# Performance work log

Hardware: AMD Instinct MI355X
Metric: run time of the kernel (lower is better)

The kernel has to match this reference:

```python
import jax, jax.numpy as jnp
import numpy as np
from jax import lax

BN_EPS = 1e-5


def setup_inputs() -> dict:
    key = jax.random.key(0)
    ks = jax.random.split(key, 12)
    h, c, i, kk = 8, 64, 96, 3
    c2, n, d = c // 2, 8, 512
    std = lambda f: np.float32(f)
    return {
        "X": jax.random.normal(ks[0], (h, n, d), jnp.float32),
        "lin_w": jax.random.normal(ks[1], (h, c2, d), jnp.float32) * std(d ** -0.5),
        "lin_b": jax.random.normal(ks[2], (h, c2), jnp.float32) * std(0.02),
        "bn_gamma": jnp.ones((h, c2), jnp.float32),
        "bn_beta": jnp.zeros((h, c2), jnp.float32),
        "px": jax.random.normal(ks[3], (1, 1, c2, 1, i), jnp.float32) * std(c ** -0.5),
        "py": jax.random.normal(ks[4], (1, 1, c2, i, 1), jnp.float32) * std(c ** -0.5),
        "kw": jax.random.normal(ks[5], (h, c, c), jnp.float32) * std(c ** -0.5),
        "kb": jax.random.normal(ks[6], (h, c), jnp.float32) * std(0.02),
        "vw": jax.random.normal(ks[7], (h, c, c), jnp.float32) * std(c ** -0.5),
        "vb": jax.random.normal(ks[8], (h, c), jnp.float32) * std(0.02),
        "sw": jax.random.normal(ks[9], (c, c, kk, kk), jnp.float32) * std((c * kk * kk) ** -0.5),
        "sb": jax.random.normal(ks[10], (c,), jnp.float32) * std(0.02),
    }


def reference(X, lin_w, lin_b, bn_gamma, bn_beta, px, py, kw, kb, vw, vb, sw, sb):
    h, n, _ = X.shape
    c = kw.shape[1]
    c2 = c // 2
    i = px.shape[-1]
    kk = sw.shape[-1]

    # --- MultiheadEmbedding: per-head Linear -> BatchNorm1d(train) -> ReLU ---
    y = jnp.einsum('hnd,hcd->hnc', X, lin_w) + lin_b[:, None, :]      # (h, n, c2)
    mu = y.mean(axis=1, keepdims=True)
    var = y.var(axis=1, keepdims=True)                                 # biased, as BN
    y = (y - mu) * lax.rsqrt(var + BN_EPS) * bn_gamma[:, None, :] + bn_beta[:, None, :]
    y = jax.nn.relu(y)
    M = jnp.transpose(y, (1, 0, 2))[..., None, None]                   # (n, h, c2, 1, 1)

    # --- PositionalEncoding: concat x/y translated copies -> (n, h, c, i, i) ---
    P = jnp.concatenate([
        jnp.broadcast_to(M + px, (n, h, c2, i, i)),
        jnp.broadcast_to(M + py, (n, h, c2, i, i)),
    ], axis=2)                                                          # (n, h, c, i, i)

    # --- TransposeAttention ---
    # grouped 1x1 key conv (groups = h)
    kp = jnp.einsum('nhcij,hdc->nhdij', P, kw) + kb[None, :, :, None, None]
    # score conv over each (c, i, i) map, shared across heads, scaled
    x = kp.reshape(n * h, c, i, i)
    s = lax.conv_general_dilated(x, sw, (1, 1), 'SAME',
                                 dimension_numbers=('NCHW', 'OIHW', 'NCHW'))
    s = (s + sb[None, :, None, None]) / np.float32((c * kk * kk) ** 0.5)
    w = jax.nn.softmax(s.reshape(n, h, c, i, i), axis=1)                # softmax over heads
    # grouped 1x1 value conv, weighted sum over heads
    vp = jnp.einsum('nhcij,hdc->nhdij', P, vw) + vb[None, :, :, None, None]
    T = (w * vp).sum(axis=1)                                            # (n, c, i, i)
    return (T, M, P, w)
```

## Files before the change

kernel.cpp:

```cpp
#include <hip/hip_runtime.h>
#include <math.h>

#define H    8
#define N    8
#define D    512
#define C    64
#define C2   32
#define I    96
#define II   9216

#define OFF_T 0
#define OFF_M 4718592
#define OFF_P 4720640
#define OFF_W 42469376

#define WS_AK 0
#define WS_AV 4096
#define WS_BK 8192
#define WS_BV 57344
#define WS_CK 106496
#define WS_CV 155648
#define WS_SS 204800
#define WS_SP 241664
#define WS_SQ 278528
#define WS_F  315392
#define WS_G2 352256
#define WS_H2 499712

__device__ __forceinline__ int bcls(int x) { return x == 0 ? 0 : (x == I - 1 ? 2 : 1); }

__global__ __launch_bounds__(256) void irf_embed(
    const float* __restrict__ X, const float* __restrict__ lin_w,
    const float* __restrict__ lin_b, const float* __restrict__ gamma,
    const float* __restrict__ beta, float* __restrict__ out)
{
    const int h = blockIdx.x, t = threadIdx.x;
    const int n = t >> 5, cc = t & 31;

    __shared__ float Xs[N * D];
    __shared__ float ys[N * C2];
    __shared__ float scale_s[C2], shift_s[C2];

    const float4* Xg  = (const float4*)(X + (size_t)h * N * D);
    float4*       Xs4 = (float4*)Xs;
    for (int idx = t; idx < N * D / 4; idx += 256) Xs4[idx] = Xg[idx];
    __syncthreads();

    const float4* wrow = (const float4*)(lin_w + ((size_t)h * C2 + cc) * D);
    const float4* xrow = (const float4*)(Xs + n * D);
    float a0 = 0.f, a1 = 0.f, a2 = 0.f, a3 = 0.f;
    #pragma unroll 4
    for (int k = 0; k < D / 4; ++k) {
        float4 xv = xrow[k], wv = wrow[k];
        a0 = fmaf(xv.x, wv.x, a0); a1 = fmaf(xv.y, wv.y, a1);
        a2 = fmaf(xv.z, wv.z, a2); a3 = fmaf(xv.w, wv.w, a3);
    }
    float y = (a0 + a1) + (a2 + a3) + lin_b[h * C2 + cc];
    ys[n * C2 + cc] = y;
    __syncthreads();

    if (t < C2) {
        float s = 0.f, ss = 0.f;
        #pragma unroll
        for (int j = 0; j < N; ++j) { float v = ys[j * C2 + t]; s += v; ss += v * v; }
        float mu  = s * (1.0f / N);
        float var = ss * (1.0f / N) - mu * mu;
        float sc  = rsqrtf(var + 1e-5f) * gamma[h * C2 + t];
        scale_s[t] = sc;
        shift_s[t] = beta[h * C2 + t] - mu * sc;
    }
    __syncthreads();

    float v = fmaxf(fmaf(y, scale_s[cc], shift_s[cc]), 0.0f);
    out[OFF_M + (n * H + h) * C2 + cc] = v;
}

__global__ __launch_bounds__(256) void irf_factors_a(
    const float* __restrict__ kw, const float* __restrict__ kb,
    const float* __restrict__ vw, const float* __restrict__ vb,
    const float* __restrict__ px, const float* __restrict__ py,
    const float* __restrict__ sw, const float* __restrict__ out,
    float* __restrict__ ws)
{
    int gid = blockIdx.x * 256 + threadIdx.x;
    if (gid < 4096) {
        int id = gid, d = id & 63, h = (id >> 6) & 7, n = id >> 9;
        const float* kwr = kw + ((size_t)h * C + d) * C;
        const float* vwr = vw + ((size_t)h * C + d) * C;
        const float* Mr  = out + OFF_M + (n * H + h) * C2;
        float ak = kb[h * C + d], av = vb[h * C + d];
        #pragma unroll 8
        for (int c = 0; c < C2; ++c) {
            float m = Mr[c];
            ak = fmaf(kwr[c] + kwr[C2 + c], m, ak);
            av = fmaf(vwr[c] + vwr[C2 + c], m, av);
        }
        ws[WS_AK + id] = ak;
        ws[WS_AV + id] = av;
    } else if (gid < 4096 + 49152) {
        int id = gid - 4096, d = id & 63, r = id >> 6, b = r % I, h = r / I;
        const float* kwr = kw + ((size_t)h * C + d) * C;
        const float* vwr = vw + ((size_t)h * C + d) * C;
        float bk = 0.f, bv = 0.f, ck = 0.f, cv = 0.f;
        #pragma unroll 8
        for (int c = 0; c < C2; ++c) {
            float pxv = px[c * I + b], pyv = py[c * I + b];
            bk = fmaf(kwr[c], pxv, bk);       bv = fmaf(vwr[c], pxv, bv);
            ck = fmaf(kwr[C2 + c], pyv, ck);  cv = fmaf(vwr[C2 + c], pyv, cv);
        }
        ws[WS_BK + id] = bk; ws[WS_BV + id] = bv;
        ws[WS_CK + id] = ck; ws[WS_CV + id] = cv;
    } else if (gid < 4096 + 49152 + 4096) {
        int id = gid - (4096 + 49152), d = id & 63, e = id >> 6;
        float k9[3][3];
        const float* swr = sw + (size_t)(e * C + d) * 9;
        #pragma unroll
        for (int p = 0; p < 3; ++p)
            #pragma unroll
            for (int q = 0; q < 3; ++q) k9[p][q] = swr[p * 3 + q];
        #pragma unroll
        for (int ra = 0; ra < 3; ++ra) {
            int pmin = (ra == 0) ? 1 : 0, pmax = (ra == 2) ? 1 : 2;
            #pragma unroll
            for (int q = 0; q < 3; ++q) {
                float sp = 0.f;
                for (int p = pmin; p <= pmax; ++p) sp += k9[p][q];
                ws[WS_SP + ((ra * 3 + q) * C + e) * C + d] = sp;
            }
            #pragma unroll
            for (int rb = 0; rb < 3; ++rb) {
                int qmin = (rb == 0) ? 1 : 0, qmax = (rb == 2) ? 1 : 2;
                float ssv = 0.f;
                for (int p = pmin; p <= pmax; ++p)
                    for (int q = qmin; q <= qmax; ++q) ssv += k9[p][q];
                ws[WS_SS + ((ra * 3 + rb) * C + e) * C + d] = ssv;
            }
        }
        #pragma unroll
        for (int rb = 0; rb < 3; ++rb) {
            int qmin = (rb == 0) ? 1 : 0, qmax = (rb == 2) ? 1 : 2;
            #pragma unroll
            for (int p = 0; p < 3; ++p) {
                float sq = 0.f;
                for (int q = qmin; q <= qmax; ++q) sq += k9[p][q];
                ws[WS_SQ + ((rb * 3 + p) * C + e) * C + d] = sq;
            }
        }
    }
}

__global__ __launch_bounds__(256) void irf_factors_b(float* __restrict__ ws)
{
    int gid = blockIdx.x * 256 + threadIdx.x;
    if (gid < 36864) {
        int id = gid, e = id & 63, h = (id >> 6) & 7, cls = (id >> 9) % 9, n = id / 4608;
        const float* ak = ws + WS_AK + (n * H + h) * C;
        const float* ss = ws + WS_SS + (cls * C + e) * C;
        float acc = 0.f;
        #pragma unroll 8
        for (int d = 0; d < C; ++d) acc = fmaf(ak[d], ss[d], acc);
        ws[WS_F + id] = acc;
    } else if (gid < 36864 + 147456) {
        int j = gid - 36864, b = j % I, e = (j / I) & 63, h = (j / (I * C)) & 7, ra = j / (I * C * H);
        int rb = bcls(b), qmin = (rb == 0) ? 1 : 0, qmax = (rb == 2) ? 1 : 2;
        float acc = 0.f;
        for (int q = qmin; q <= qmax; ++q) {
            const float* sp = ws + WS_SP + ((ra * 3 + q) * C + e) * C;
            const float* bk = ws + WS_BK + ((h * I) + (b + q - 1)) * C;
            #pragma unroll 8
            for (int d = 0; d < C; ++d) acc = fmaf(sp[d], bk[d], acc);
        }
        ws[WS_G2 + j] = acc;
    } else if (gid < 36864 + 2 * 147456) {
        int j = gid - 36864 - 147456, e = j & 63, h = (j >> 6) & 7, rb = (j >> 9) % 3, a = j / 1536;
        int ra = bcls(a), pmin = (ra == 0) ? 1 : 0, pmax = (ra == 2) ? 1 : 2;
        float acc = 0.f;
        for (int p = pmin; p <= pmax; ++p) {
            const float* sq = ws + WS_SQ + ((rb * 3 + p) * C + e) * C;
            const float* ck = ws + WS_CK + ((h * I) + (a + p - 1)) * C;
            #pragma unroll 8
            for (int d = 0; d < C; ++d) acc = fmaf(sq[d], ck[d], acc);
        }
        ws[WS_H2 + j] = acc;
    }
}

__global__ __launch_bounds__(256) void irf_site(
    const float* __restrict__ px, const float* __restrict__ py,
    const float* __restrict__ sb, const float* __restrict__ ws,
    float* __restrict__ out)
{
    const int bid = blockIdx.x;
    const int n = bid / I, a = bid - n * I;
    const int ra = bcls(a);
    const int t = threadIdx.x;
    const int e8 = t >> 5, bl = t & 31;

    __shared__ float Fs[3 * 512];
    __shared__ float H2s[3 * 512];
    __shared__ float Avs[512];
    __shared__ float Cvs[512];
    __shared__ float Ms_[256];
    __shared__ float pys[C2];
    __shared__ float sbs[C];

    {
        const float* fsrc = ws + WS_F + (n * 9 + ra * 3) * 512;
        const float* hsrc = ws + WS_H2 + a * 1536;
        for (int o = t; o < 1536; o += 256) { Fs[o] = fsrc[o]; H2s[o] = hsrc[o]; }
        const float* avsrc = ws + WS_AV + n * 512;
        for (int o = t; o < 512; o += 256) {
            Avs[o] = avsrc[o];
            int h = o >> 6, e = o & 63;
            Cvs[o] = ws[WS_CV + ((h * I) + a) * C + e];
        }
        const float* msrc = out + OFF_M + n * 256;
        if (t < 256) Ms_[t] = msrc[t];
        if (t < C2)  pys[t] = py[t * I + a];
        if (t < C)   sbs[t] = sb[t];
    }
    __syncthreads();

    const float inv24 = 1.0f / 24.0f;

    for (int eb = 0; eb < 8; ++eb) {
        int e = eb * 8 + e8;
        float sbe = sbs[e];
        for (int bc = 0; bc < 3; ++bc) {
            int b = bc * 32 + bl;
            int rb = bcls(b);
            float sv[H];
            float mx = -1e30f;
            #pragma unroll
            for (int h = 0; h < H; ++h) {
                float s = Fs[rb * 512 + h * 64 + e] + H2s[rb * 512 + h * 64 + e]
                        + ws[WS_G2 + ((ra * H + h) * C + e) * I + b] + sbe;
                sv[h] = s * inv24;
                mx = fmaxf(mx, sv[h]);
            }
            float sum = 0.f;
            #pragma unroll
            for (int h = 0; h < H; ++h) { sv[h] = __expf(sv[h] - mx); sum += sv[h]; }
            float rs = 1.0f / sum;
            float T = 0.f;
            #pragma unroll
            for (int h = 0; h < H; ++h) {
                float w = sv[h] * rs;
                out[OFF_W + (size_t)(((n * H + h) * C + e) * I + a) * I + b] = w;
                float vp = Avs[h * 64 + e] + Cvs[h * 64 + e]
                         + ws[WS_BV + ((h * I) + b) * C + e];
                T = fmaf(w, vp, T);
            }
            out[OFF_T + (size_t)((n * C + e) * I + a) * I + b] = T;
        }
    }

    for (int h = 0; h < H; ++h) {
        for (int cb = 0; cb < 8; ++cb) {
            int c = cb * 8 + e8;
            float base = (c < C2) ? Ms_[h * C2 + c] : (Ms_[h * C2 + c - C2] + pys[c - C2]);
            bool use_px = (c < C2);
            for (int bc = 0; bc < 3; ++bc) {
                int b = bc * 32 + bl;
                float val = use_px ? (base + px[c * I + b]) : base;
                out[OFF_P + (size_t)(((n * H + h) * C + c) * I + a) * I + b] = val;
            }
        }
    }
}

extern "C" void kernel_launch(void* const* d_in, const int* in_sizes, int n_in,
                              void* d_out, int out_size, void* d_ws, size_t ws_size,
                              hipStream_t stream) {
    const float* X     = (const float*)d_in[0];
    const float* lin_w = (const float*)d_in[1];
    const float* lin_b = (const float*)d_in[2];
    const float* gamma = (const float*)d_in[3];
    const float* beta  = (const float*)d_in[4];
    const float* px    = (const float*)d_in[5];
    const float* py    = (const float*)d_in[6];
    const float* kw    = (const float*)d_in[7];
    const float* kb    = (const float*)d_in[8];
    const float* vw    = (const float*)d_in[9];
    const float* vb    = (const float*)d_in[10];
    const float* sw    = (const float*)d_in[11];
    const float* sb    = (const float*)d_in[12];

    float* out = (float*)d_out;
    float* ws  = (float*)d_ws;

    irf_embed    <<<8,    256, 0, stream>>>(X, lin_w, lin_b, gamma, beta, out);
    irf_factors_a<<<224,  256, 0, stream>>>(kw, kb, vw, vb, px, py, sw, out, ws);
    irf_factors_b<<<1296, 256, 0, stream>>>(ws);
    irf_site     <<<768,  256, 0, stream>>>(px, py, sb, ws, out);
}
```

Measured before the change: 482.4 us.

## Vectorize irf_site stores with float4, transpose BV layout, prefold score terms

The main site kernel now has each thread handle four consecutive b positions and write W, T and P as float4, replacing scalar stores. The BV workspace is stored b-contiguous so its reads can also be float4. F, H2 and the score bias are summed into one shared array, as are Av and Cv, and px is staged in shared memory. The goal is fewer, wider global memory transactions on this store-bound kernel. In exchange each thread holds more registers for the float4 softmax state, and the b-boundary class handling now assumes only the first and last float4 groups differ.

After: 413.5 us. 1.17x faster.

```diff
diff --git a/kernel.cpp b/kernel.cpp
--- a/kernel.cpp
+++ b/kernel.cpp
@@ -108,7 +108,8 @@
             bk = fmaf(kwr[c], pxv, bk);       bv = fmaf(vwr[c], pxv, bv);
             ck = fmaf(kwr[C2 + c], pyv, ck);  cv = fmaf(vwr[C2 + c], pyv, cv);
         }
-        ws[WS_BK + id] = bk; ws[WS_BV + id] = bv;
+        ws[WS_BK + id] = bk;
+        ws[WS_BV + (h * C + d) * I + b] = bv;
         ws[WS_CK + id] = ck; ws[WS_CV + id] = cv;
     } else if (gid < 4096 + 49152 + 4096) {
         int id = gid - (4096 + 49152), d = id & 63, e = id >> 6;
@@ -194,78 +195,99 @@
     const int n = bid / I, a = bid - n * I;
     const int ra = bcls(a);
     const int t = threadIdx.x;
-    const int e8 = t >> 5, bl = t & 31;
-
-    __shared__ float Fs[3 * 512];
-    __shared__ float H2s[3 * 512];
-    __shared__ float Avs[512];
-    __shared__ float Cvs[512];
+
+    __shared__ float FH[3 * 512];
+    __shared__ float AC[512];
     __shared__ float Ms_[256];
+    __shared__ float pxs[C2 * I];
     __shared__ float pys[C2];
-    __shared__ float sbs[C];
 
     {
         const float* fsrc = ws + WS_F + (n * 9 + ra * 3) * 512;
         const float* hsrc = ws + WS_H2 + a * 1536;
-        for (int o = t; o < 1536; o += 256) { Fs[o] = fsrc[o]; H2s[o] = hsrc[o]; }
+        for (int o = t; o < 1536; o += 256) FH[o] = fsrc[o] + hsrc[o] + sb[o & 63];
         const float* avsrc = ws + WS_AV + n * 512;
         for (int o = t; o < 512; o += 256) {
-            Avs[o] = avsrc[o];
             int h = o >> 6, e = o & 63;
-            Cvs[o] = ws[WS_CV + ((h * I) + a) * C + e];
-        }
-        const float* msrc = out + OFF_M + n * 256;
-        if (t < 256) Ms_[t] = msrc[t];
-        if (t < C2)  pys[t] = py[t * I + a];
-        if (t < C)   sbs[t] = sb[t];
+            AC[o] = avsrc[o] + ws[WS_CV + ((h * I) + a) * C + e];
+        }
+        Ms_[t] = out[OFF_M + n * 256 + t];
+        for (int o = t; o < C2 * I; o += 256) pxs[o] = px[o];
+        if (t < C2) pys[t] = py[t * I + a];
     }
     __syncthreads();
 
     const float inv24 = 1.0f / 24.0f;
 
-    for (int eb = 0; eb < 8; ++eb) {
-        int e = eb * 8 + e8;
-        float sbe = sbs[e];
-        for (int bc = 0; bc < 3; ++bc) {
-            int b = bc * 32 + bl;
-            int rb = bcls(b);
-            float sv[H];
-            float mx = -1e30f;
-            #pragma unroll
-            for (int h = 0; h < H; ++h) {
-                float s = Fs[rb * 512 + h * 64 + e] + H2s[rb * 512 + h * 64 + e]
-                        + ws[WS_G2 + ((ra * H + h) * C + e) * I + b] + sbe;
-                sv[h] = s * inv24;
-                mx = fmaxf(mx, sv[h]);
-            }
-            float sum = 0.f;
-            #pragma unroll
-            for (int h = 0; h < H; ++h) { sv[h] = __expf(sv[h] - mx); sum += sv[h]; }
-            float rs = 1.0f / sum;
-            float T = 0.f;
-            #pragma unroll
-            for (int h = 0; h < H; ++h) {
-                float w = sv[h] * rs;
-                out[OFF_W + (size_t)(((n * H + h) * C + e) * I + a) * I + b] = w;
-                float vp = Avs[h * 64 + e] + Cvs[h * 64 + e]
-                         + ws[WS_BV + ((h * I) + b) * C + e];
-                T = fmaf(w, vp, T);
-            }
-            out[OFF_T + (size_t)((n * C + e) * I + a) * I + b] = T;
-        }
-    }
-
-    for (int h = 0; h < H; ++h) {
-        for (int cb = 0; cb < 8; ++cb) {
-            int c = cb * 8 + e8;
-            float base = (c < C2) ? Ms_[h * C2 + c] : (Ms_[h * C2 + c - C2] + pys[c - C2]);
-            bool use_px = (c < C2);
-            for (int bc = 0; bc < 3; ++bc) {
-                int b = bc * 32 + bl;
-                float val = use_px ? (base + px[c * I + b]) : base;
-                out[OFF_P + (size_t)(((n * H + h) * C + c) * I + a) * I + b] = val;
-            }
-        }
+    #pragma unroll
+    for (int it = 0; it < 6; ++it) {
+        int idx = it * 256 + t;
+        int e = idx / 24, b4 = idx - e * 24;
+        int b = b4 * 4;
+
+        float4 sv[H];
+        float4 mx = make_float4(-1e30f, -1e30f, -1e30f, -1e30f);
+        #pragma unroll
+        for (int h = 0; h < H; ++h) {
+            float4 g2 = ((const float4*)(ws + WS_G2 + ((ra * H + h) * C + e) * I))[b4];
+            float fh1 = FH[512 + h * 64 + e];
+            float fx = fh1, fw = fh1;
+            if (b4 == 0)  fx = FH[h * 64 + e];
+            if (b4 == 23) fw = FH[1024 + h * 64 + e];
+            float4 s;
+            s.x = (fx  + g2.x) * inv24;
+            s.y = (fh1 + g2.y) * inv24;
+            s.z = (fh1 + g2.z) * inv24;
+            s.w = (fw  + g2.w) * inv24;
+            sv[h] = s;
+            mx.x = fmaxf(mx.x, s.x); mx.y = fmaxf(mx.y, s.y);
+            mx.z = fmaxf(mx.z, s.z); mx.w = fmaxf(mx.w, s.w);
+        }
+        float4 sum = make_float4(0.f, 0.f, 0.f, 0.f);
+        #pragma unroll
+        for (int h = 0; h < H; ++h) {
+            sv[h].x = __expf(sv[h].x - mx.x); sum.x += sv[h].x;
+            sv[h].y = __expf(sv[h].y - mx.y); sum.y += sv[h].y;
+            sv[h].z = __expf(sv[h].z - mx.z); sum.z += sv[h].z;
+            sv[h].w = __expf(sv[h].w - mx.w); sum.w += sv[h].w;
+        }
+        float4 rs;
+        rs.x = 1.0f / sum.x; rs.y = 1.0f / sum.y;
+        rs.z = 1.0f / sum.z; rs.w = 1.0f / sum.w;
+
+        float4 T = make_float4(0.f, 0.f, 0.f, 0.f);
+        #pragma unroll
+        for (int h = 0; h < H; ++h) {
+            float4 w;
+            w.x = sv[h].x * rs.x; w.y = sv[h].y * rs.y;
+            w.z = sv[h].z * rs.z; w.w = sv[h].w * rs.w;
+            ((float4*)(out + OFF_W + (size_t)(((n * H + h) * C + e) * I + a) * I))[b4] = w;
+            float ac = AC[h * 64 + e];
+            float4 bv = ((const float4*)(ws + WS_BV + (h * C + e) * I))[b4];
+            T.x = fmaf(w.x, ac + bv.x, T.x);
+            T.y = fmaf(w.y, ac + bv.y, T.y);
+            T.z = fmaf(w.z, ac + bv.z, T.z);
+            T.w = fmaf(w.w, ac + bv.w, T.w);
+        }
+        ((float4*)(out + OFF_T + (size_t)((n * C + e) * I + a) * I))[b4] = T;
+    }
+
+    #pragma unroll
+    for (int it = 0; it < 48; ++it) {
+        int idx = it * 256 + t;
+        int b4 = idx % 24, rem = idx / 24;
+        int c = rem & 63, h = rem >> 6;
+        float4 v;
+        if (c < C2) {
+            float base = Ms_[h * C2 + c];
+            float4 p4 = ((const float4*)(pxs + c * I))[b4];
+            v.x = base + p4.x; v.y = base + p4.y;
+            v.z = base + p4.z; v.w = base + p4.w;
+        } else {
+            float bb = Ms_[h * C2 + c - C2] + pys[c - C2];
+            v = make_float4(bb, bb, bb, bb);
+        }
+        ((float4*)(out + OFF_P + (size_t)(((n * H + h) * C + c) * I + a) * I))[b4] = v;
     }
 }
 
```
